# Kernel optimization log

Measured on AMD Instinct MI355X. Metric: run time of the kernel, lower is better.

## Reference

```python
import jax, jax.numpy as jnp
import numpy as np

B_, T_, DIN, H, DZ, DX = 64, 256, 128, 256, 8, 8


def setup_inputs() -> dict:
    key = jax.random.key(0)
    ks = jax.random.split(key, 13)
    p = lambda k, sh: jax.random.normal(k, sh, dtype=jnp.float32) * 0.05
    return {
        "y": jax.random.normal(ks[0], (B_, T_, DIN), dtype=jnp.float32),
        "W_ih": p(ks[1], (3 * H, DIN)), "W_hh": p(ks[2], (3 * H, H)),
        "b_ih": p(ks[3], (3 * H,)), "b_hh": p(ks[4], (3 * H,)),
        "W_mz": p(ks[5], (DZ, H)), "b_mz": p(ks[6], (DZ,)),
        "W_mx": p(ks[7], (DX, H)), "b_mx": p(ks[8], (DX,)),
        "W_pz": p(ks[9], (2 * DZ, H)), "b_pz": p(ks[10], (2 * DZ,)),
        "W_cx": p(ks[11], (DX * DX, H)), "b_cx": p(ks[12], (DX * DX,)),
    }


def _gru(y, W_ih, W_hh, b_ih, b_hh):
    # torch nn.GRU (single layer, unidirectional, batch_first)
    B, T, _ = y.shape
    Hh = W_hh.shape[1]
    x_proj = jnp.einsum('btd,gd->btg', y, W_ih) + b_ih  # [B,T,3H]

    def step(h, xp):
        hp = h @ W_hh.T + b_hh
        xr, xz, xn = jnp.split(xp, 3, axis=-1)
        hr, hz, hn = jnp.split(hp, 3, axis=-1)
        r = jax.nn.sigmoid(xr + hr)
        z = jax.nn.sigmoid(xz + hz)
        n = jnp.tanh(xn + r * hn)
        h_new = (1.0 - z) * n + z * h
        return h_new, h_new

    h0 = jnp.zeros((B, Hh), dtype=y.dtype)
    _, hs = jax.lax.scan(step, h0, jnp.swapaxes(x_proj, 0, 1))
    return jnp.swapaxes(hs, 0, 1)  # [B,T,H]


def _forward(y, W_ih, W_hh, b_ih, b_hh, W_mz, b_mz, W_mx, b_mx, W_pz, b_pz, W_cx, b_cx):
    enc = _gru(y, W_ih, W_hh, b_ih, b_hh)                       # [B,T,H]
    mean_z = enc @ W_mz.T + b_mz                                 # [B,T,DZ]
    mean_x = enc @ W_mx.T + b_mx                                 # [B,T,DX]
    bd_z = enc @ W_pz.T + b_pz                                   # [B,T,2*DZ]  (apply_softplus=False)

    # banded cov: per latent dim, upper-bidiagonal cholesky factor [B,T,T]
    diag = jnp.moveaxis(jax.nn.softplus(bd_z[..., :DZ]), -1, 0)  # [DZ,B,T]
    off = jnp.moveaxis(bd_z[:, :-1, DZ:], -1, 0)                 # [DZ,B,T-1]
    B, T = diag.shape[1], diag.shape[2]
    idx = jnp.arange(T)
    chol_z = (jnp.zeros((DZ, B, T, T), dtype=y.dtype)
              .at[:, :, idx, idx].set(diag)
              .at[:, :, idx[:-1], idx[1:]].set(off))             # [DZ,B,T,T]

    # anchor first two x-dims at t=0 (in-place mutation in torch)
    mean_x = mean_x.at[:, :, :2].add(-mean_x[:, 0:1, :2])
    mean_x_flat = mean_x.reshape(B * T, DX)

    cov_x = enc @ W_cx.T + b_cx                                  # [B,T,DX*DX]
    cov_x_flat = cov_x.reshape(B * T, DX, DX)
    return mean_z, chol_z, mean_x_flat, cov_x_flat


def reference(y, W_ih, W_hh, b_ih, b_hh, W_mz, b_mz, W_mx, b_mx, W_pz, b_pz, W_cx, b_cx):
    return _forward(y, W_ih, W_hh, b_ih, b_hh, W_mz, b_mz, W_mx, b_mx, W_pz, b_pz, W_cx, b_cx)
```

## Files before the change

### kernel.cpp

```cpp
#include <hip/hip_runtime.h>
#include <cstdint>
#include <cstddef>

#define B_   64
#define T_   256
#define DIN_ 128
#define H_   256
#define G3_  768

typedef _Float16 f16x8 __attribute__((ext_vector_type(8)));
typedef float    f32x4 __attribute__((ext_vector_type(4)));

#define MFMA(a, b, c) __builtin_amdgcn_mfma_f32_16x16x32_f16((a), (b), (c), 0, 0, 0)

__device__ __forceinline__ unsigned short f2h(float f) {
  _Float16 h = (_Float16)f;
  return __builtin_bit_cast(unsigned short, h);
}

__global__ __launch_bounds__(256) void prep_kernel(
    const float* __restrict__ W_ih, const float* __restrict__ W_hh,
    const float* __restrict__ W_mz, const float* __restrict__ W_mx,
    const float* __restrict__ W_pz, const float* __restrict__ W_cx,
    float* __restrict__ WT_ih, float* __restrict__ WheadT,
    unsigned* __restrict__ Wreg) {
  int i = blockIdx.x * 256 + threadIdx.x;
  if (i < 98304) {
    int k = i / 768, g = i % 768;
    WT_ih[i] = W_ih[g * 128 + k];
  } else if (i < 98304 + 24576) {
    int j = i - 98304;
    int c = j >> 8, k = j & 255;
    float v;
    if (c < 8)       v = W_mz[c * 256 + k];
    else if (c < 16) v = W_mx[(c - 8) * 256 + k];
    else if (c < 32) v = W_pz[(c - 16) * 256 + k];
    else             v = W_cx[(c - 32) * 256 + k];
    WheadT[j] = v;
  } else {
    int m = i - 122880;
    int d = m & 3, n = m >> 2;
    int tid = n & 1023, fi = n >> 10;
    int g  = fi >> 3, kf = fi & 7;
    int wv = tid >> 6, l = tid & 63;
    int u = wv * 16 + (l & 15);
    int k = kf * 32 + ((l >> 4) << 3) + 2 * d;
    int row = g * 256 + u;
    unsigned short lo = f2h(W_hh[row * 256 + k]);
    unsigned short hi = f2h(W_hh[row * 256 + k + 1]);
    Wreg[m] = ((unsigned)hi << 16) | (unsigned)lo;
  }
}

__global__ __launch_bounds__(256) void xproj_kernel(
    const float* __restrict__ y, const float* __restrict__ WT_ih,
    const float* __restrict__ b_ih, const float* __restrict__ b_hh,
    float* __restrict__ xp) {
  __shared__ float ylds[64][132];
  int tid = threadIdx.x;
  int row0 = (blockIdx.x >> 1) * 64;
  int c0 = (blockIdx.x & 1) * 3;
  const float4* y4 = (const float4*)(y + (size_t)row0 * DIN_);
#pragma unroll
  for (int i = 0; i < 8; ++i) {
    int idx = i * 256 + tid;
    float4 v = y4[idx];
    int r = idx >> 5, c4 = (idx & 31) * 4;
    ylds[r][c4 + 0] = v.x; ylds[r][c4 + 1] = v.y;
    ylds[r][c4 + 2] = v.z; ylds[r][c4 + 3] = v.w;
  }
  __syncthreads();
  int tx = tid & 15, ty = tid >> 4;
  for (int c = c0; c < c0 + 3; ++c) {
    int col0 = c * 128 + tx * 8;
    float acc[4][8];
#pragma unroll
    for (int a = 0; a < 4; ++a)
#pragma unroll
      for (int b = 0; b < 8; ++b) acc[a][b] = 0.f;
#pragma unroll 4
    for (int k = 0; k < 128; ++k) {
      float4 w0 = *(const float4*)&WT_ih[k * 768 + col0];
      float4 w1 = *(const float4*)&WT_ih[k * 768 + col0 + 4];
      float a0 = ylds[ty * 4 + 0][k], a1 = ylds[ty * 4 + 1][k];
      float a2 = ylds[ty * 4 + 2][k], a3 = ylds[ty * 4 + 3][k];
      acc[0][0] += a0 * w0.x; acc[0][1] += a0 * w0.y; acc[0][2] += a0 * w0.z; acc[0][3] += a0 * w0.w;
      acc[0][4] += a0 * w1.x; acc[0][5] += a0 * w1.y; acc[0][6] += a0 * w1.z; acc[0][7] += a0 * w1.w;
      acc[1][0] += a1 * w0.x; acc[1][1] += a1 * w0.y; acc[1][2] += a1 * w0.z; acc[1][3] += a1 * w0.w;
      acc[1][4] += a1 * w1.x; acc[1][5] += a1 * w1.y; acc[1][6] += a1 * w1.z; acc[1][7] += a1 * w1.w;
      acc[2][0] += a2 * w0.x; acc[2][1] += a2 * w0.y; acc[2][2] += a2 * w0.z; acc[2][3] += a2 * w0.w;
      acc[2][4] += a2 * w1.x; acc[2][5] += a2 * w1.y; acc[2][6] += a2 * w1.z; acc[2][7] += a2 * w1.w;
      acc[3][0] += a3 * w0.x; acc[3][1] += a3 * w0.y; acc[3][2] += a3 * w0.z; acc[3][3] += a3 * w0.w;
      acc[3][4] += a3 * w1.x; acc[3][5] += a3 * w1.y; acc[3][6] += a3 * w1.z; acc[3][7] += a3 * w1.w;
    }
    float4 b0 = *(const float4*)&b_ih[col0];
    float4 b1 = *(const float4*)&b_ih[col0 + 4];
    if (c < 4) {
      float4 h0 = *(const float4*)&b_hh[col0];
      float4 h1 = *(const float4*)&b_hh[col0 + 4];
      b0.x += h0.x; b0.y += h0.y; b0.z += h0.z; b0.w += h0.w;
      b1.x += h1.x; b1.y += h1.y; b1.z += h1.z; b1.w += h1.w;
    }
#pragma unroll
    for (int a = 0; a < 4; ++a) {
      int row = row0 + ty * 4 + a;
      float4 o0, o1;
      o0.x = acc[a][0] + b0.x; o0.y = acc[a][1] + b0.y; o0.z = acc[a][2] + b0.z; o0.w = acc[a][3] + b0.w;
      o1.x = acc[a][4] + b1.x; o1.y = acc[a][5] + b1.y; o1.z = acc[a][6] + b1.z; o1.w = acc[a][7] + b1.w;
      *(float4*)&xp[(size_t)row * G3_ + col0] = o0;
      *(float4*)&xp[(size_t)row * G3_ + col0 + 4] = o1;
    }
  }
}

__global__ __launch_bounds__(1024) void gru_kernel(
    const float* __restrict__ xp, const unsigned* __restrict__ Wreg,
    const float* __restrict__ b_hh, float* enc, float4* __restrict__ cholU) {
  int tid = threadIdx.x;
  int b = blockIdx.x;
  if (b >= 64) {
    float4 zz = {0.f, 0.f, 0.f, 0.f};
    int idx = (b - 64) * 1024 + tid;
    for (; idx < 4194304; idx += 98304) cholU[idx] = zz;
    return;
  }
  int w = tid >> 6;
  int l = tid & 63;
  int g16 = l >> 4;
  int u = w * 16 + (l & 15);
  __shared__ alignas(16) unsigned short h16[2][256];

  f16x8 wfR[8], wfZ[8], wfN[8];
  const uint4* W4 = (const uint4*)Wreg;
#pragma unroll
  for (int kf = 0; kf < 8; ++kf) {
    wfR[kf] = __builtin_bit_cast(f16x8, W4[(0 * 8 + kf) * 1024 + tid]);
    wfZ[kf] = __builtin_bit_cast(f16x8, W4[(1 * 8 + kf) * 1024 + tid]);
    wfN[kf] = __builtin_bit_cast(f16x8, W4[(2 * 8 + kf) * 1024 + tid]);
  }
  if (tid < 32) {
    uint4 z = {0u, 0u, 0u, 0u};
    ((uint4*)h16)[tid] = z;
  }
  const float* xpb = xp + (size_t)b * (T_ * G3_);
  float* encb = enc + (size_t)b * (T_ * H_);
  float bhn = b_hh[512 + u];
  float hold = 0.f;
  const f32x4 z4 = {0.f, 0.f, 0.f, 0.f};
  __syncthreads();
  const uint4* h4 = (const uint4*)h16;
  for (int t = 0; t < T_; ++t) {
    asm volatile("" ::: "memory");
    const float* xq = xpb + (size_t)t * G3_;
    float xr = xq[u], xz = xq[256 + u], xn = xq[512 + u];
    int cur = t & 1;
    f32x4 aR, aZ, aN;
    {
      uint4 hq = h4[cur * 32 + g16];
      f16x8 hk = __builtin_bit_cast(f16x8, hq);
      aR = MFMA(hk, wfR[0], z4);
      aZ = MFMA(hk, wfZ[0], z4);
      aN = MFMA(hk, wfN[0], z4);
    }
#pragma unroll
    for (int kf = 1; kf < 8; ++kf) {
      uint4 hq = h4[cur * 32 + kf * 4 + g16];
      f16x8 hk = __builtin_bit_cast(f16x8, hq);
      aR = MFMA(hk, wfR[kf], aR);
      aZ = MFMA(hk, wfZ[kf], aZ);
      aN = MFMA(hk, wfN[kf], aN);
    }
    float pr = aR[0] + xr, pz = aZ[0] + xz;
    float r_ = 1.f / (1.f + __expf(-pr));
    float q_ = 1.f / (1.f + __expf(-pz));
    float zh = q_ * hold, om = 1.f - q_;
    float pn = aN[0] + bhn;
    float a = xn + r_ * pn;
    a = fminf(15.f, fmaxf(-15.f, a));
    float e = __expf(2.f * a);
    float n = (e - 1.f) / (e + 1.f);
    float hn = om * n + zh;
    hold = hn;
    if (g16 == 0) {
      encb[t * H_ + u] = hn;
      h16[cur ^ 1][u] = f2h(hn);
    }
    __syncthreads();
  }
}

__global__ __launch_bounds__(384) void heads_kernel(
    const float* __restrict__ enc, const float* __restrict__ WheadT,
    const float* __restrict__ b_mz, const float* __restrict__ b_mx,
    const float* __restrict__ b_pz, const float* __restrict__ b_cx,
    float* __restrict__ out_meanz, float* __restrict__ out_meanx,
    float* __restrict__ out_covx, float* __restrict__ stage,
    float* __restrict__ chol, float* __restrict__ anchor,
    const float* __restrict__ W_mx) {
  int tid = threadIdx.x;
  if (blockIdx.x >= 512) {
    __shared__ float red[4];
    int bid = blockIdx.x - 512;
    int b = bid >> 1, d = bid & 1;
    if (tid < 256) {
      float v = enc[(size_t)b * (T_ * H_) + tid] * W_mx[d * 256 + tid];
#pragma unroll
      for (int off = 32; off >= 1; off >>= 1) v += __shfl_down(v, off, 64);
      if ((tid & 63) == 0) red[tid >> 6] = v;
    }
    __syncthreads();
    if (tid == 0)
      anchor[b * 2 + d] = b_mx[d] + ((red[0] + red[1]) + (red[2] + red[3]));
    return;
  }
  __shared__ float el[32 * 256];
  int row0 = blockIdx.x * 32;
  const float4* e4 = (const float4*)(enc + (size_t)row0 * 256);
  float4* el4 = (float4*)el;
#pragma unroll
  for (int i = 0; i < 6; ++i) {
    int idx = i * 384 + tid;
    if (idx < 2048) el4[idx] = e4[idx];
  }
  __syncthreads();
  int rg = tid / 96, c = tid - rg * 96;
  const float4* Wc = (const float4*)(WheadT + c * 256);
  float acc[8];
#pragma unroll
  for (int r = 0; r < 8; ++r) acc[r] = 0.f;
  for (int k4 = 0; k4 < 64; ++k4) {
    float4 w4 = Wc[k4];
#pragma unroll
    for (int r = 0; r < 8; ++r) {
      float4 ev = el4[(rg * 8 + r) * 64 + k4];
      acc[r] += w4.x * ev.x; acc[r] += w4.y * ev.y;
      acc[r] += w4.z * ev.z; acc[r] += w4.w * ev.w;
    }
  }
#pragma unroll
  for (int r = 0; r < 8; ++r) {
    int row = row0 + rg * 8 + r;
    float a_ = acc[r];
    if (c < 8) {
      out_meanz[(size_t)row * 8 + c] = a_ + b_mz[c];
    } else if (c < 16) {
      int d = c - 8;
      out_meanx[(size_t)row * 8 + d] = a_ + b_mx[d];
    } else if (c < 32) {
      int d = c - 16;
      float v = a_ + b_pz[d];
      if (d < 8)
        v = (v > 0.f) ? (v + log1pf(__expf(-v))) : log1pf(__expf(v));
      int bb = row >> 8, tt = row & 255;
      if (d < 4) {
        stage[(size_t)row * 16 + d] = v;
      } else if (d < 8) {
        chol[(((size_t)d * 64 + bb) * 256 + tt) * 256 + tt] = v;
      } else if (d < 12) {
        stage[(size_t)row * 16 + d] = v;
      } else {
        int dd = d - 8;
        if (tt < 255)
          chol[(((size_t)dd * 64 + bb) * 256 + tt) * 256 + tt + 1] = v;
      }
    } else {
      int d = c - 32;
      out_covx[(size_t)row * 64 + d] = a_ + b_cx[d];
    }
  }
}

__global__ __launch_bounds__(256) void chol_fin(
    const float* __restrict__ stage, float4* __restrict__ chol,
    const float* __restrict__ anchor, float* __restrict__ mean_x) {
  int i = blockIdx.x * 256 + threadIdx.x;
  int stride = gridDim.x * 256;
  for (; i < 4227072; i += stride) {
    if (i < 4194304) {
      int d = i >> 20;
      int bt = (i >> 6) & 16383;
      int t = bt & 255;
      int lane = i & 63;
      float vd = 0.f, vo = 0.f;
      if ((t >> 2) == lane)       vd = stage[bt * 16 + d];
      if (((t + 1) >> 2) == lane) vo = stage[bt * 16 + 8 + d];
      int te = t & 3, oe = (t + 1) & 3;
      float4 v;
      v.x = (te == 0 ? vd : 0.f) + (oe == 0 ? vo : 0.f);
      v.y = (te == 1 ? vd : 0.f) + (oe == 1 ? vo : 0.f);
      v.z = (te == 2 ? vd : 0.f) + (oe == 2 ? vo : 0.f);
      v.w = (te == 3 ? vd : 0.f) + (oe == 3 ? vo : 0.f);
      chol[i] = v;
    } else {
      int j2 = i - 4194304;
      int row = j2 >> 1, d = j2 & 1;
      mean_x[(size_t)row * 8 + d] -= anchor[(row >> 8) * 2 + d];
    }
  }
}

extern "C" void kernel_launch(void* const* d_in, const int* in_sizes, int n_in,
                              void* d_out, int out_size, void* d_ws, size_t ws_size,
                              hipStream_t stream) {
  const float* y    = (const float*)d_in[0];
  const float* W_ih = (const float*)d_in[1];
  const float* W_hh = (const float*)d_in[2];
  const float* b_ih = (const float*)d_in[3];
  const float* b_hh = (const float*)d_in[4];
  const float* W_mz = (const float*)d_in[5];
  const float* b_mz = (const float*)d_in[6];
  const float* W_mx = (const float*)d_in[7];
  const float* b_mx = (const float*)d_in[8];
  const float* W_pz = (const float*)d_in[9];
  const float* b_pz = (const float*)d_in[10];
  const float* W_cx = (const float*)d_in[11];
  const float* b_cx = (const float*)d_in[12];

  float* out    = (float*)d_out;
  float* mean_z = out;
  float* chol   = out + 131072;
  float* mean_x = out + 33685504;
  float* cov_x  = out + 33816576;

  float* ws      = (float*)d_ws;
  float* WT_ih   = ws;
  float* WheadT  = ws + 98304;
  unsigned* Wreg = (unsigned*)(ws + 122880);
  float* anchor  = ws + 221184;
  float* stage   = ws + 221312;

  float* xp  = chol;
  float* enc = chol + 12582912;

  prep_kernel<<<864, 256, 0, stream>>>(W_ih, W_hh, W_mz, W_mx, W_pz, W_cx,
                                       WT_ih, WheadT, Wreg);
  xproj_kernel<<<512, 256, 0, stream>>>(y, WT_ih, b_ih, b_hh, xp);
  gru_kernel<<<160, 1024, 0, stream>>>(xp, Wreg, b_hh, enc,
                                       ((float4*)chol) + 4194304);
  heads_kernel<<<640, 384, 0, stream>>>(enc, WheadT, b_mz, b_mx, b_pz, b_cx,
                                        mean_z, mean_x, cov_x, stage,
                                        chol, anchor, W_mx);
  chol_fin<<<4096, 256, 0, stream>>>(stage, (float4*)chol, anchor, mean_x);
}
```

Before: 547.4 us.

## Fuse banded Cholesky fill and anchor into heads kernel; split GRU MFMA chains

The heads kernel now stages the diagonal and off-diagonal values for the first four latent dims in LDS and writes the full dense float4 Cholesky rows itself. It also computes the t=0 anchor from its LDS copy of the encoder rows. This removes the separate chol_fill pass, the global staging buffer, and the extra 128 anchor blocks; the trailing kernel now only subtracts the anchor from mean_x. In the GRU loop each gate's 8-deep MFMA chain is split into two 4-deep accumulators, and the second half of the N-gate chain is issued after the sigmoid work. This is meant to shorten the serial MFMA dependency on every timestep. The fused chol writes overwrite the d=3 region that aliases enc, which is safe only because each block writes over exactly the enc rows it has already copied into LDS.

```diff
diff --git a/kernel.cpp b/kernel.cpp
--- a/kernel.cpp
+++ b/kernel.cpp
@@ -154,27 +154,33 @@
     const float* xq = xpb + (size_t)t * G3_;
     float xr = xq[u], xz = xq[256 + u], xn = xq[512 + u];
     int cur = t & 1;
-    f32x4 aR, aZ, aN;
-    {
-      uint4 hq = h4[cur * 32 + g16];
-      f16x8 hk = __builtin_bit_cast(f16x8, hq);
-      aR = MFMA(hk, wfR[0], z4);
-      aZ = MFMA(hk, wfZ[0], z4);
-      aN = MFMA(hk, wfN[0], z4);
-    }
-#pragma unroll
-    for (int kf = 1; kf < 8; ++kf) {
-      uint4 hq = h4[cur * 32 + kf * 4 + g16];
-      f16x8 hk = __builtin_bit_cast(f16x8, hq);
-      aR = MFMA(hk, wfR[kf], aR);
-      aZ = MFMA(hk, wfZ[kf], aZ);
-      aN = MFMA(hk, wfN[kf], aN);
-    }
-    float pr = aR[0] + xr, pz = aZ[0] + xz;
+    const uint4* hb = h4 + cur * 32 + g16;
+    f16x8 h0 = __builtin_bit_cast(f16x8, hb[0]);
+    f16x8 h1 = __builtin_bit_cast(f16x8, hb[4]);
+    f16x8 h2 = __builtin_bit_cast(f16x8, hb[8]);
+    f16x8 h3 = __builtin_bit_cast(f16x8, hb[12]);
+    f32x4 aR0 = MFMA(h0, wfR[0], z4); aR0 = MFMA(h1, wfR[1], aR0);
+    aR0 = MFMA(h2, wfR[2], aR0);      aR0 = MFMA(h3, wfR[3], aR0);
+    f32x4 aZ0 = MFMA(h0, wfZ[0], z4); aZ0 = MFMA(h1, wfZ[1], aZ0);
+    aZ0 = MFMA(h2, wfZ[2], aZ0);      aZ0 = MFMA(h3, wfZ[3], aZ0);
+    f32x4 aN0 = MFMA(h0, wfN[0], z4); aN0 = MFMA(h1, wfN[1], aN0);
+    aN0 = MFMA(h2, wfN[2], aN0);      aN0 = MFMA(h3, wfN[3], aN0);
+    f16x8 h4_ = __builtin_bit_cast(f16x8, hb[16]);
+    f16x8 h5  = __builtin_bit_cast(f16x8, hb[20]);
+    f16x8 h6  = __builtin_bit_cast(f16x8, hb[24]);
+    f16x8 h7  = __builtin_bit_cast(f16x8, hb[28]);
+    f32x4 aR1 = MFMA(h4_, wfR[4], z4); aR1 = MFMA(h5, wfR[5], aR1);
+    aR1 = MFMA(h6, wfR[6], aR1);       aR1 = MFMA(h7, wfR[7], aR1);
+    f32x4 aZ1 = MFMA(h4_, wfZ[4], z4); aZ1 = MFMA(h5, wfZ[5], aZ1);
+    aZ1 = MFMA(h6, wfZ[6], aZ1);       aZ1 = MFMA(h7, wfZ[7], aZ1);
+    float pr = (aR0[0] + aR1[0]) + xr;
+    float pz = (aZ0[0] + aZ1[0]) + xz;
     float r_ = 1.f / (1.f + __expf(-pr));
     float q_ = 1.f / (1.f + __expf(-pz));
     float zh = q_ * hold, om = 1.f - q_;
-    float pn = aN[0] + bhn;
+    f32x4 aN1 = MFMA(h4_, wfN[4], z4); aN1 = MFMA(h5, wfN[5], aN1);
+    aN1 = MFMA(h6, wfN[6], aN1);       aN1 = MFMA(h7, wfN[7], aN1);
+    float pn = (aN0[0] + aN1[0]) + bhn;
     float a = xn + r_ * pn;
     a = fminf(15.f, fmaxf(-15.f, a));
     float e = __expf(2.f * a);
@@ -194,26 +200,12 @@
     const float* __restrict__ b_mz, const float* __restrict__ b_mx,
     const float* __restrict__ b_pz, const float* __restrict__ b_cx,
     float* __restrict__ out_meanz, float* __restrict__ out_meanx,
-    float* __restrict__ out_covx, float* __restrict__ stage,
-    float* __restrict__ chol, float* __restrict__ anchor,
-    const float* __restrict__ W_mx) {
+    float* __restrict__ out_covx, float* __restrict__ chol,
+    float* __restrict__ anchor, const float* __restrict__ W_mx) {
+  __shared__ float el[32 * 256];
+  __shared__ float dsd[32][4], dso[32][4];
+  __shared__ float redA[4], redB[4];
   int tid = threadIdx.x;
-  if (blockIdx.x >= 512) {
-    __shared__ float red[4];
-    int bid = blockIdx.x - 512;
-    int b = bid >> 1, d = bid & 1;
-    if (tid < 256) {
-      float v = enc[(size_t)b * (T_ * H_) + tid] * W_mx[d * 256 + tid];
-#pragma unroll
-      for (int off = 32; off >= 1; off >>= 1) v += __shfl_down(v, off, 64);
-      if ((tid & 63) == 0) red[tid >> 6] = v;
-    }
-    __syncthreads();
-    if (tid == 0)
-      anchor[b * 2 + d] = b_mx[d] + ((red[0] + red[1]) + (red[2] + red[3]));
-    return;
-  }
-  __shared__ float el[32 * 256];
   int row0 = blockIdx.x * 32;
   const float4* e4 = (const float4*)(enc + (size_t)row0 * 256);
   float4* el4 = (float4*)el;
@@ -239,7 +231,8 @@
   }
 #pragma unroll
   for (int r = 0; r < 8; ++r) {
-    int row = row0 + rg * 8 + r;
+    int lr = rg * 8 + r;
+    int row = row0 + lr;
     float a_ = acc[r];
     if (c < 8) {
       out_meanz[(size_t)row * 8 + c] = a_ + b_mz[c];
@@ -253,11 +246,11 @@
         v = (v > 0.f) ? (v + log1pf(__expf(-v))) : log1pf(__expf(v));
       int bb = row >> 8, tt = row & 255;
       if (d < 4) {
-        stage[(size_t)row * 16 + d] = v;
+        dsd[lr][d] = v;
       } else if (d < 8) {
         chol[(((size_t)d * 64 + bb) * 256 + tt) * 256 + tt] = v;
       } else if (d < 12) {
-        stage[(size_t)row * 16 + d] = v;
+        dso[lr][d - 8] = v;
       } else {
         int dd = d - 8;
         if (tt < 255)
@@ -268,35 +261,47 @@
       out_covx[(size_t)row * 64 + d] = a_ + b_cx[d];
     }
   }
+  bool anch = (row0 & 255) == 0;
+  if (anch && tid < 256) {
+    float e0 = el[tid];
+    float va0 = e0 * W_mx[tid];
+    float va1 = e0 * W_mx[256 + tid];
+#pragma unroll
+    for (int off = 32; off >= 1; off >>= 1) {
+      va0 += __shfl_down(va0, off, 64);
+      va1 += __shfl_down(va1, off, 64);
+    }
+    if ((tid & 63) == 0) { redA[tid >> 6] = va0; redB[tid >> 6] = va1; }
+  }
+  __syncthreads();
+  if (anch && tid == 0) {
+    int b = row0 >> 8;
+    anchor[b * 2 + 0] = b_mx[0] + ((redA[0] + redA[1]) + (redA[2] + redA[3]));
+    anchor[b * 2 + 1] = b_mx[1] + ((redB[0] + redB[1]) + (redB[2] + redB[3]));
+  }
+  float4* chol4 = (float4*)chol;
+  for (int idx = tid; idx < 8192; idx += 384) {
+    int j = idx & 63, lr = (idx >> 6) & 31, d = idx >> 11;
+    int grow = row0 + lr;
+    int bb = grow >> 8, tt = grow & 255;
+    int jd = tt >> 2, jo = (tt + 1) >> 2;
+    float vd = (j == jd) ? dsd[lr][d] : 0.f;
+    float vo = (j == jo) ? dso[lr][d] : 0.f;
+    int te = tt & 3, oe = (tt + 1) & 3;
+    float4 v;
+    v.x = (te == 0 ? vd : 0.f) + (oe == 0 ? vo : 0.f);
+    v.y = (te == 1 ? vd : 0.f) + (oe == 1 ? vo : 0.f);
+    v.z = (te == 2 ? vd : 0.f) + (oe == 2 ? vo : 0.f);
+    v.w = (te == 3 ? vd : 0.f) + (oe == 3 ? vo : 0.f);
+    chol4[(((size_t)d * 64 + bb) * 256 + tt) * 64 + j] = v;
+  }
 }
 
 __global__ __launch_bounds__(256) void chol_fin(
-    const float* __restrict__ stage, float4* __restrict__ chol,
     const float* __restrict__ anchor, float* __restrict__ mean_x) {
-  int i = blockIdx.x * 256 + threadIdx.x;
-  int stride = gridDim.x * 256;
-  for (; i < 4227072; i += stride) {
-    if (i < 4194304) {
-      int d = i >> 20;
-      int bt = (i >> 6) & 16383;
-      int t = bt & 255;
-      int lane = i & 63;
-      float vd = 0.f, vo = 0.f;
-      if ((t >> 2) == lane)       vd = stage[bt * 16 + d];
-      if (((t + 1) >> 2) == lane) vo = stage[bt * 16 + 8 + d];
-      int te = t & 3, oe = (t + 1) & 3;
-      float4 v;
-      v.x = (te == 0 ? vd : 0.f) + (oe == 0 ? vo : 0.f);
-      v.y = (te == 1 ? vd : 0.f) + (oe == 1 ? vo : 0.f);
-      v.z = (te == 2 ? vd : 0.f) + (oe == 2 ? vo : 0.f);
-      v.w = (te == 3 ? vd : 0.f) + (oe == 3 ? vo : 0.f);
-      chol[i] = v;
-    } else {
-      int j2 = i - 4194304;
-      int row = j2 >> 1, d = j2 & 1;
-      mean_x[(size_t)row * 8 + d] -= anchor[(row >> 8) * 2 + d];
-    }
-  }
+  int j = blockIdx.x * 256 + threadIdx.x;
+  int row = j >> 1, d = j & 1;
+  mean_x[(size_t)row * 8 + d] -= anchor[(row >> 8) * 2 + d];
 }
 
 extern "C" void kernel_launch(void* const* d_in, const int* in_sizes, int n_in,
@@ -327,7 +332,6 @@
   float* WheadT  = ws + 98304;
   unsigned* Wreg = (unsigned*)(ws + 122880);
   float* anchor  = ws + 221184;
-  float* stage   = ws + 221312;
 
   float* xp  = chol;
   float* enc = chol + 12582912;
@@ -337,8 +341,8 @@
   xproj_kernel<<<512, 256, 0, stream>>>(y, WT_ih, b_ih, b_hh, xp);
   gru_kernel<<<160, 1024, 0, stream>>>(xp, Wreg, b_hh, enc,
                                        ((float4*)chol) + 4194304);
-  heads_kernel<<<640, 384, 0, stream>>>(enc, WheadT, b_mz, b_mx, b_pz, b_cx,
-                                        mean_z, mean_x, cov_x, stage,
-                                        chol, anchor, W_mx);
-  chol_fin<<<4096, 256, 0, stream>>>(stage, (float4*)chol, anchor, mean_x);
-}
+  heads_kernel<<<512, 384, 0, stream>>>(enc, WheadT, b_mz, b_mx, b_pz, b_cx,
+                                        mean_z, mean_x, cov_x, chol,
+                                        anchor, W_mx);
+  chol_fin<<<128, 256, 0, stream>>>(anchor, mean_x);
+}
```

After: 763.1 us. 1.39x slower.
